# Optimization experiments

Hardware: AMD Instinct MI355X
Metric: run time of the kernel (lower is better)

Reference implementation:

```python
import jax, jax.numpy as jnp
import numpy as np

EXPERT_CAPACITY = 1024  # per-batch per-expert capacity (token_priority <= capacity)


def setup_inputs() -> dict:
    key = jax.random.key(0)
    ks = jax.random.split(key, 5)
    B, S, D, FF, E = 2, 4096, 1024, 4096, 8
    return {
        "hidden_states": jax.random.normal(ks[0], (B, S, D), dtype=jnp.float32),
        "gate_w": jax.random.normal(ks[1], (D, E), dtype=jnp.float32) * (1.0 / np.sqrt(D)),
        "w1": jax.random.normal(ks[2], (E, D, FF), dtype=jnp.float32) * (1.0 / np.sqrt(D)),
        "w2": jax.random.normal(ks[3], (E, FF, D), dtype=jnp.float32) * (1.0 / np.sqrt(FF)),
        "w3": jax.random.normal(ks[4], (E, D, FF), dtype=jnp.float32) * (1.0 / np.sqrt(D)),
    }


def reference(hidden_states, gate_w, w1, w2, w3):
    B, S, D = hidden_states.shape
    E = gate_w.shape[1]
    C = EXPERT_CAPACITY

    # ---- route (jitter_noise = 0) ----
    router_logits = jnp.einsum("bsd,de->bse", hidden_states, gate_w)  # [B,S,E]
    router_probs = jax.nn.softmax(router_logits, axis=-1)
    sel = jnp.argmax(router_probs, axis=-1)  # [B,S] top-1 expert
    onehot = jax.nn.one_hot(sel, E, dtype=jnp.int32)  # [B,S,E]
    priority = jnp.cumsum(onehot, axis=1)  # cumsum over sequence (dim=-2)
    # position of token in its chosen expert's buffer (0-based)
    pos = jnp.take_along_axis(priority, sel[..., None], axis=-1)[..., 0] - 1  # [B,S]
    keep = pos < C  # token_priority <= expert_capacity
    max_prob = jnp.max(router_probs, axis=-1, keepdims=True)  # [B,S,1]

    # ---- dispatch: scatter kept tokens into [B,E,C,D]; dropped tokens have pos>=C -> mode='drop'
    b_idx = jnp.broadcast_to(jnp.arange(B)[:, None], (B, S))
    buf = jnp.zeros((B, E, C, D), dtype=hidden_states.dtype)
    buf = buf.at[b_idx, sel, pos].set(hidden_states, mode="drop")

    # ---- per-expert gated MLP (grouped GEMM): act(x@w1) * (x@w3) @ w2 ----
    g = jax.nn.silu(jnp.einsum("becd,edf->becf", buf, w1))
    u = jnp.einsum("becd,edf->becf", buf, w3)
    expert_out = jnp.einsum("becf,efd->becd", g * u, w2)  # [B,E,C,D]

    # ---- combine: kept tokens get expert output, dropped tokens keep hidden_states ----
    pos_g = jnp.minimum(pos, C - 1)  # safe gather index for dropped tokens
    gathered = expert_out[b_idx, sel, pos_g]  # [B,S,D]
    next_states = jnp.where(keep[..., None], gathered, hidden_states)
    out = max_prob * next_states  # dropout is identity (p=0)
    return out, router_logits
```

## Files before the change

kernel.cpp:

```cpp
#include <hip/hip_runtime.h>
#include <hip/hip_bf16.h>
#include <stdint.h>

#define B_  2
#define S_  4096
#define D_  1024
#define FF_ 4096
#define E_  8
#define C_  1024

typedef unsigned short u16;
typedef unsigned int   u32;
typedef float f32x4  __attribute__((ext_vector_type(4)));
typedef short bf16x8 __attribute__((ext_vector_type(8)));
typedef u16   u16x8  __attribute__((ext_vector_type(8)));

static __device__ __forceinline__ u16 f2bf(float f) {
    union { float f; u32 u; } v; v.f = f;
    u32 u = v.u;
    u32 r = (u + 0x7FFFu + ((u >> 16) & 1u)) >> 16;
    return (u16)r;
}

static __device__ __forceinline__ void gload_lds16(const u16* g, u16* l) {
    __builtin_amdgcn_global_load_lds(
        (const __attribute__((address_space(1))) u32*)g,
        (__attribute__((address_space(3))) u32*)l, 16, 0, 0);
}

__global__ __launch_bounds__(256) void cvt_hidden(const float* __restrict__ src,
                                                  u16* __restrict__ dst, int n8) {
    int i = blockIdx.x * 256 + threadIdx.x;
    if (i >= n8) return;
    const float4* s = (const float4*)src + (size_t)i * 2;
    float4 a = s[0], b = s[1];
    u16x8 o;
    o[0] = f2bf(a.x); o[1] = f2bf(a.y); o[2] = f2bf(a.z); o[3] = f2bf(a.w);
    o[4] = f2bf(b.x); o[5] = f2bf(b.y); o[6] = f2bf(b.z); o[7] = f2bf(b.w);
    *((u16x8*)dst + i) = o;
}

__global__ __launch_bounds__(256) void transpose_cvt(const float* __restrict__ src,
                                                     u16* __restrict__ dst, int K, int N) {
    __shared__ float tile[32][33];
    size_t mat = (size_t)blockIdx.z * K * N;
    int n0 = blockIdx.x * 32, k0 = blockIdx.y * 32;
    int tx = threadIdx.x & 31, ty = threadIdx.x >> 5;
#pragma unroll
    for (int i = 0; i < 32; i += 8)
        tile[ty + i][tx] = src[mat + (size_t)(k0 + ty + i) * N + n0 + tx];
    __syncthreads();
#pragma unroll
    for (int i = 0; i < 32; i += 8)
        dst[mat + (size_t)(n0 + ty + i) * K + k0 + tx] = f2bf(tile[tx][ty + i]);
}

__global__ __launch_bounds__(256) void router_kernel(const float* __restrict__ hidden,
                                                     const float* __restrict__ gate_w,
                                                     float* __restrict__ logits_out,
                                                     int* __restrict__ sel,
                                                     float* __restrict__ maxp) {
    __shared__ float gw[D_ * E_];
    for (int i = threadIdx.x; i < D_ * E_ / 4; i += 256)
        ((float4*)gw)[i] = ((const float4*)gate_w)[i];
    __syncthreads();

    int wave = threadIdx.x >> 6, lane = threadIdx.x & 63;
    int tok = blockIdx.x * 4 + wave;
    const float* hrow = hidden + (size_t)tok * D_;

    double acc[8] = {0, 0, 0, 0, 0, 0, 0, 0};
#pragma unroll 4
    for (int i = 0; i < D_ / 64; i++) {
        int d = i * 64 + lane;
        float h = hrow[d];
        const float4* g4 = (const float4*)(gw + d * 8);
        float4 g0 = g4[0], g1 = g4[1];
        acc[0] += (double)h * g0.x; acc[1] += (double)h * g0.y;
        acc[2] += (double)h * g0.z; acc[3] += (double)h * g0.w;
        acc[4] += (double)h * g1.x; acc[5] += (double)h * g1.y;
        acc[6] += (double)h * g1.z; acc[7] += (double)h * g1.w;
    }
#pragma unroll
    for (int off = 32; off > 0; off >>= 1)
#pragma unroll
        for (int e = 0; e < 8; e++)
            acc[e] += __shfl_xor(acc[e], off);

    float l[8];
#pragma unroll
    for (int e = 0; e < 8; e++) l[e] = (float)acc[e];
    if (lane < 8) logits_out[(size_t)tok * 8 + lane] = l[lane];

    int am = 0; float mx = l[0];
#pragma unroll
    for (int e = 1; e < 8; e++) if (l[e] > mx) { mx = l[e]; am = e; }
    float sum = 0.f;
#pragma unroll
    for (int e = 0; e < 8; e++) sum += expf(l[e] - mx);
    if (lane == 0) { sel[tok] = am; maxp[tok] = 1.0f / sum; }
}

__global__ void scan_kernel(const int* __restrict__ sel, int* __restrict__ pos,
                            int* __restrict__ slot_token, int* __restrict__ counts) {
    int wave = threadIdx.x >> 6, lane = threadIdx.x & 63;
    int b = wave;
    int carry[8] = {0, 0, 0, 0, 0, 0, 0, 0};
    unsigned long long below = (lane == 0) ? 0ull : ((~0ull) >> (64 - lane));
    for (int s0 = 0; s0 < S_; s0 += 64) {
        int s = s0 + lane;
        int e = sel[b * S_ + s];
        int p = 0;
#pragma unroll
        for (int ex = 0; ex < 8; ex++) {
            unsigned long long m = __ballot(e == ex);
            if (e == ex) p = carry[ex] + (int)__popcll(m & below);
            carry[ex] += (int)__popcll(m);
        }
        pos[b * S_ + s] = p;
        if (p < C_) slot_token[(b * E_ + e) * C_ + p] = s;
    }
    if (lane < 8) {
        int c = carry[lane];
        counts[b * E_ + lane] = c < C_ ? c : C_;
    }
}

__global__ __launch_bounds__(256) void gemm1_kernel(const u16* __restrict__ x,
                                                    const u16* __restrict__ w1t,
                                                    const u16* __restrict__ w3t,
                                                    const int* __restrict__ slot_token,
                                                    const int* __restrict__ counts,
                                                    u16* __restrict__ hbuf) {
    int z = blockIdx.z;
    int cnt = counts[z];
    int c0 = blockIdx.y * 128;
    if (c0 >= cnt) return;
    int n0 = blockIdx.x * 64;
    int b = z >> 3, e = z & 7;

    __shared__ u16 As[128 * 64];
    __shared__ u16 B1s[64 * 64];
    __shared__ u16 B3s[64 * 64];

    int tid = threadIdx.x, wave = tid >> 6, lane = tid & 63;
    int wr = wave >> 1, wc = wave & 1;

    const u16* a_src[4];
#pragma unroll
    for (int i = 0; i < 4; i++) {
        int chunk = wave * 4 + i;
        int row = chunk * 8 + (lane >> 3);
        int slot = c0 + row;
        int s = (slot < cnt) ? slot_token[z * C_ + slot] : 0;
        int srcslot = (lane & 7) ^ (row & 7);
        a_src[i] = x + ((size_t)(b * S_ + s)) * D_ + srcslot * 8;
    }
    const u16 *b1_src[2], *b3_src[2];
#pragma unroll
    for (int i = 0; i < 2; i++) {
        int chunk = wave * 2 + i;
        int row = chunk * 8 + (lane >> 3);
        int srcslot = (lane & 7) ^ (row & 7);
        size_t off = ((size_t)e * FF_ + n0 + row) * D_ + srcslot * 8;
        b1_src[i] = w1t + off;
        b3_src[i] = w3t + off;
    }

    f32x4 acc1[4][2] = {};
    f32x4 acc3[4][2] = {};

    for (int k0 = 0; k0 < D_; k0 += 64) {
#pragma unroll
        for (int i = 0; i < 4; i++)
            gload_lds16(a_src[i] + k0, As + (wave * 4 + i) * 512);
#pragma unroll
        for (int i = 0; i < 2; i++) {
            gload_lds16(b1_src[i] + k0, B1s + (wave * 2 + i) * 512);
            gload_lds16(b3_src[i] + k0, B3s + (wave * 2 + i) * 512);
        }
        __syncthreads();
#pragma unroll
        for (int kk = 0; kk < 2; kk++) {
            bf16x8 af[4];
#pragma unroll
            for (int fm = 0; fm < 4; fm++) {
                int row = wr * 64 + fm * 16 + (lane & 15);
                int sl = (kk * 4 + (lane >> 4)) ^ (row & 7);
                af[fm] = *(const bf16x8*)(As + row * 64 + sl * 8);
            }
            bf16x8 b1f[2], b3f[2];
#pragma unroll
            for (int fn = 0; fn < 2; fn++) {
                int nl = wc * 32 + fn * 16 + (lane & 15);
                int sl = (kk * 4 + (lane >> 4)) ^ (nl & 7);
                b1f[fn] = *(const bf16x8*)(B1s + nl * 64 + sl * 8);
                b3f[fn] = *(const bf16x8*)(B3s + nl * 64 + sl * 8);
            }
#pragma unroll
            for (int fm = 0; fm < 4; fm++)
#pragma unroll
                for (int fn = 0; fn < 2; fn++) {
                    acc1[fm][fn] = __builtin_amdgcn_mfma_f32_16x16x32_bf16(af[fm], b1f[fn], acc1[fm][fn], 0, 0, 0);
                    acc3[fm][fn] = __builtin_amdgcn_mfma_f32_16x16x32_bf16(af[fm], b3f[fn], acc3[fm][fn], 0, 0, 0);
                }
        }
        __syncthreads();
    }

#pragma unroll
    for (int fm = 0; fm < 4; fm++) {
        int rbase = c0 + wr * 64 + fm * 16 + ((lane >> 4) << 2);
#pragma unroll
        for (int fn = 0; fn < 2; fn++) {
            int col = n0 + wc * 32 + fn * 16 + (lane & 15);
#pragma unroll
            for (int r = 0; r < 4; r++) {
                int slot = rbase + r;
                if (slot < cnt) {
                    float g = acc1[fm][fn][r];
                    float u = acc3[fm][fn][r];
                    float h = (g / (1.f + __expf(-g))) * u;
                    hbuf[((size_t)z * C_ + slot) * FF_ + col] = f2bf(h);
                }
            }
        }
    }
}

__global__ __launch_bounds__(256) void gemm2_kernel(const u16* __restrict__ hbuf,
                                                    const u16* __restrict__ w2t,
                                                    const int* __restrict__ slot_token,
                                                    const int* __restrict__ counts,
                                                    const float* __restrict__ maxp,
                                                    float* __restrict__ out) {
    int z = blockIdx.z;
    int cnt = counts[z];
    int c0 = blockIdx.y * 128;
    if (c0 >= cnt) return;
    int n0 = blockIdx.x * 128;
    int b = z >> 3, e = z & 7;

    __shared__ u16 As[128 * 64];
    __shared__ u16 Bs[128 * 64];

    int tid = threadIdx.x, wave = tid >> 6, lane = tid & 63;
    int wr = wave >> 1, wc = wave & 1;

    const u16 *a_src[4], *b_src[4];
#pragma unroll
    for (int i = 0; i < 4; i++) {
        int chunk = wave * 4 + i;
        int row = chunk * 8 + (lane >> 3);
        int srcslot = (lane & 7) ^ (row & 7);
        a_src[i] = hbuf + ((size_t)z * C_ + c0 + row) * FF_ + srcslot * 8;
        b_src[i] = w2t + ((size_t)e * D_ + n0 + row) * FF_ + srcslot * 8;
    }

    f32x4 acc[4][4] = {};

    for (int k0 = 0; k0 < FF_; k0 += 64) {
#pragma unroll
        for (int i = 0; i < 4; i++) {
            gload_lds16(a_src[i] + k0, As + (wave * 4 + i) * 512);
            gload_lds16(b_src[i] + k0, Bs + (wave * 4 + i) * 512);
        }
        __syncthreads();
#pragma unroll
        for (int kk = 0; kk < 2; kk++) {
            bf16x8 af[4], bfv[4];
#pragma unroll
            for (int fm = 0; fm < 4; fm++) {
                int row = wr * 64 + fm * 16 + (lane & 15);
                int sl = (kk * 4 + (lane >> 4)) ^ (row & 7);
                af[fm] = *(const bf16x8*)(As + row * 64 + sl * 8);
            }
#pragma unroll
            for (int fn = 0; fn < 4; fn++) {
                int nl = wc * 64 + fn * 16 + (lane & 15);
                int sl = (kk * 4 + (lane >> 4)) ^ (nl & 7);
                bfv[fn] = *(const bf16x8*)(Bs + nl * 64 + sl * 8);
            }
#pragma unroll
            for (int fm = 0; fm < 4; fm++)
#pragma unroll
                for (int fn = 0; fn < 4; fn++)
                    acc[fm][fn] = __builtin_amdgcn_mfma_f32_16x16x32_bf16(af[fm], bfv[fn], acc[fm][fn], 0, 0, 0);
        }
        __syncthreads();
    }

#pragma unroll
    for (int fm = 0; fm < 4; fm++) {
        int rbase = c0 + wr * 64 + fm * 16 + ((lane >> 4) << 2);
#pragma unroll
        for (int r = 0; r < 4; r++) {
            int slot = rbase + r;
            if (slot < cnt) {
                int s = slot_token[z * C_ + slot];
                float sc = maxp[b * S_ + s];
                float* orow = out + ((size_t)b * S_ + s) * D_;
#pragma unroll
                for (int fn = 0; fn < 4; fn++) {
                    int col = n0 + wc * 64 + fn * 16 + (lane & 15);
                    orow[col] = sc * acc[fm][fn][r];
                }
            }
        }
    }
}

__global__ __launch_bounds__(256) void combine_dropped(const float* __restrict__ hidden,
                                                       const int* __restrict__ pos,
                                                       const float* __restrict__ maxp,
                                                       float* __restrict__ out) {
    int t = blockIdx.x;
    if (pos[t] < C_) return;
    float sc = maxp[t];
    const float* src = hidden + (size_t)t * D_;
    float* dst = out + (size_t)t * D_;
    for (int d = threadIdx.x; d < D_; d += 256) dst[d] = sc * src[d];
}

extern "C" void kernel_launch(void* const* d_in, const int* in_sizes, int n_in,
                              void* d_out, int out_size, void* d_ws, size_t ws_size,
                              hipStream_t stream) {
    const float* hidden = (const float*)d_in[0];
    const float* gate_w = (const float*)d_in[1];
    const float* w1     = (const float*)d_in[2];
    const float* w2     = (const float*)d_in[3];
    const float* w3     = (const float*)d_in[4];

    float* out        = (float*)d_out;
    float* logits_out = out + (size_t)B_ * S_ * D_;

    char* ws = (char*)d_ws;
    u16* hidden_bf = (u16*)ws;            ws += (size_t)B_ * S_ * D_ * 2;
    u16* w1t       = (u16*)ws;            ws += (size_t)E_ * D_ * FF_ * 2;
    u16* w3t       = (u16*)ws;            ws += (size_t)E_ * D_ * FF_ * 2;
    u16* w2t       = (u16*)ws;            ws += (size_t)E_ * D_ * FF_ * 2;
    u16* hbuf      = (u16*)ws;            ws += (size_t)B_ * E_ * C_ * FF_ * 2;
    int*   sel        = (int*)ws;         ws += (size_t)B_ * S_ * 4;
    int*   pos        = (int*)ws;         ws += (size_t)B_ * S_ * 4;
    float* maxp       = (float*)ws;       ws += (size_t)B_ * S_ * 4;
    int*   slot_token = (int*)ws;         ws += (size_t)B_ * E_ * C_ * 4;
    int*   counts     = (int*)ws;         ws += (size_t)B_ * E_ * 4;

    cvt_hidden<<<(B_ * S_ * D_ / 8 + 255) / 256, 256, 0, stream>>>(hidden, hidden_bf, B_ * S_ * D_ / 8);
    transpose_cvt<<<dim3(FF_ / 32, D_ / 32, E_), 256, 0, stream>>>(w1, w1t, D_, FF_);
    transpose_cvt<<<dim3(FF_ / 32, D_ / 32, E_), 256, 0, stream>>>(w3, w3t, D_, FF_);
    transpose_cvt<<<dim3(D_ / 32, FF_ / 32, E_), 256, 0, stream>>>(w2, w2t, FF_, D_);

    router_kernel<<<B_ * S_ / 4, 256, 0, stream>>>(hidden, gate_w, logits_out, sel, maxp);
    scan_kernel<<<1, 128, 0, stream>>>(sel, pos, slot_token, counts);

    gemm1_kernel<<<dim3(FF_ / 64, C_ / 128, B_ * E_), 256, 0, stream>>>(hidden_bf, w1t, w3t, slot_token, counts, hbuf);
    gemm2_kernel<<<dim3(D_ / 128, C_ / 128, B_ * E_), 256, 0, stream>>>(hbuf, w2t, slot_token, counts, maxp, out);
    combine_dropped<<<B_ * S_, 256, 0, stream>>>(hidden, pos, maxp, out);
}
```

Before: 574.8 us.

## Double-buffer grouped GEMMs, widen gemm1 tile, fuse bf16 cast into router

Both expert GEMMs now use double-buffered LDS with a K-step of 32, prefetching the next stage before computing the current one. They sync with raw s_waitcnt and s_barrier and raise wave priority around the MFMA block. gemm1 widens its N tile from 64 to 128 to reuse each A tile more. The hidden-state bf16 conversion is folded into the router kernel, and the weight transpose uses 64x64 tiles with vectorized loads and stores and an XOR-swizzled LDS layout. The aim is to hide global-load latency, cut launches and improve transpose bandwidth, at the cost of more registers and LDS, which may reduce occupancy.

Result: slower. 609.5 us (+6.0%).

```diff
diff --git a/kernel.cpp b/kernel.cpp
--- a/kernel.cpp
+++ b/kernel.cpp
@@ -28,38 +28,48 @@
         (__attribute__((address_space(3))) u32*)l, 16, 0, 0);
 }
 
-__global__ __launch_bounds__(256) void cvt_hidden(const float* __restrict__ src,
-                                                  u16* __restrict__ dst, int n8) {
-    int i = blockIdx.x * 256 + threadIdx.x;
-    if (i >= n8) return;
-    const float4* s = (const float4*)src + (size_t)i * 2;
-    float4 a = s[0], b = s[1];
-    u16x8 o;
-    o[0] = f2bf(a.x); o[1] = f2bf(a.y); o[2] = f2bf(a.z); o[3] = f2bf(a.w);
-    o[4] = f2bf(b.x); o[5] = f2bf(b.y); o[6] = f2bf(b.z); o[7] = f2bf(b.w);
-    *((u16x8*)dst + i) = o;
-}
+#define BAR()    asm volatile("s_barrier" ::: "memory")
+#define WAITV(n) asm volatile("s_waitcnt vmcnt(" #n ")" ::: "memory")
 
 __global__ __launch_bounds__(256) void transpose_cvt(const float* __restrict__ src,
                                                      u16* __restrict__ dst, int K, int N) {
-    __shared__ float tile[32][33];
+    __shared__ u16 t[64 * 64];
     size_t mat = (size_t)blockIdx.z * K * N;
-    int n0 = blockIdx.x * 32, k0 = blockIdx.y * 32;
-    int tx = threadIdx.x & 31, ty = threadIdx.x >> 5;
-#pragma unroll
-    for (int i = 0; i < 32; i += 8)
-        tile[ty + i][tx] = src[mat + (size_t)(k0 + ty + i) * N + n0 + tx];
+    int n0 = blockIdx.x * 64, k0 = blockIdx.y * 64;
+    int l = threadIdx.x & 63, w = threadIdx.x >> 6;
+#pragma unroll
+    for (int p = 0; p < 2; ++p) {
+        int k = p * 32 + w * 8 + ((l >> 4) << 1);
+        int n = (l & 15) * 4;
+        float4 v0 = *(const float4*)&src[mat + (size_t)(k0 + k) * N + n0 + n];
+        float4 v1 = *(const float4*)&src[mat + (size_t)(k0 + k + 1) * N + n0 + n];
+        float a0[4] = {v0.x, v0.y, v0.z, v0.w};
+        float a1[4] = {v1.x, v1.y, v1.z, v1.w};
+#pragma unroll
+        for (int j = 0; j < 4; ++j) {
+            int nn = n + j;
+            u32 pk = (u32)f2bf(a0[j]) | ((u32)f2bf(a1[j]) << 16);
+            int slot = (k >> 3) ^ ((nn & 7) ^ ((nn >> 3) & 7));
+            *(u32*)((char*)t + nn * 128 + slot * 16 + (k & 7) * 2) = pk;
+        }
+    }
     __syncthreads();
 #pragma unroll
-    for (int i = 0; i < 32; i += 8)
-        dst[mat + (size_t)(n0 + ty + i) * K + k0 + tx] = f2bf(tile[tx][ty + i]);
+    for (int p = 0; p < 2; ++p) {
+        int n = p * 32 + (threadIdx.x >> 3);
+        int k8 = threadIdx.x & 7;
+        int slot = k8 ^ ((n & 7) ^ ((n >> 3) & 7));
+        u16x8 v = *(u16x8*)((char*)t + n * 128 + slot * 16);
+        *(u16x8*)&dst[mat + (size_t)(n0 + n) * K + k0 + k8 * 8] = v;
+    }
 }
 
 __global__ __launch_bounds__(256) void router_kernel(const float* __restrict__ hidden,
                                                      const float* __restrict__ gate_w,
                                                      float* __restrict__ logits_out,
                                                      int* __restrict__ sel,
-                                                     float* __restrict__ maxp) {
+                                                     float* __restrict__ maxp,
+                                                     u16* __restrict__ xbf) {
     __shared__ float gw[D_ * E_];
     for (int i = threadIdx.x; i < D_ * E_ / 4; i += 256)
         ((float4*)gw)[i] = ((const float4*)gate_w)[i];
@@ -68,12 +78,14 @@
     int wave = threadIdx.x >> 6, lane = threadIdx.x & 63;
     int tok = blockIdx.x * 4 + wave;
     const float* hrow = hidden + (size_t)tok * D_;
+    u16* xrow = xbf + (size_t)tok * D_;
 
     double acc[8] = {0, 0, 0, 0, 0, 0, 0, 0};
 #pragma unroll 4
     for (int i = 0; i < D_ / 64; i++) {
         int d = i * 64 + lane;
         float h = hrow[d];
+        xrow[d] = f2bf(h);
         const float4* g4 = (const float4*)(gw + d * 8);
         float4 g0 = g4[0], g1 = g4[1];
         acc[0] += (double)h * g0.x; acc[1] += (double)h * g0.y;
@@ -136,90 +148,99 @@
     int cnt = counts[z];
     int c0 = blockIdx.y * 128;
     if (c0 >= cnt) return;
-    int n0 = blockIdx.x * 64;
+    int n0 = blockIdx.x * 128;
     int b = z >> 3, e = z & 7;
 
-    __shared__ u16 As[128 * 64];
-    __shared__ u16 B1s[64 * 64];
-    __shared__ u16 B3s[64 * 64];
-
-    int tid = threadIdx.x, wave = tid >> 6, lane = tid & 63;
-    int wr = wave >> 1, wc = wave & 1;
-
-    const u16* a_src[4];
-#pragma unroll
-    for (int i = 0; i < 4; i++) {
-        int chunk = wave * 4 + i;
-        int row = chunk * 8 + (lane >> 3);
-        int slot = c0 + row;
-        int s = (slot < cnt) ? slot_token[z * C_ + slot] : 0;
-        int srcslot = (lane & 7) ^ (row & 7);
-        a_src[i] = x + ((size_t)(b * S_ + s)) * D_ + srcslot * 8;
-    }
-    const u16 *b1_src[2], *b3_src[2];
+    __shared__ u16 lds[2 * 12288];
+
+    int tid = threadIdx.x, w = tid >> 6, l = tid & 63;
+    int wr = w >> 1, wc = w & 1;
+
+    const u16 *aptr[2], *b1ptr[2], *b3ptr[2];
+    int sbase[2];
 #pragma unroll
     for (int i = 0; i < 2; i++) {
-        int chunk = wave * 2 + i;
-        int row = chunk * 8 + (lane >> 3);
-        int srcslot = (lane & 7) ^ (row & 7);
-        size_t off = ((size_t)e * FF_ + n0 + row) * D_ + srcslot * 8;
-        b1_src[i] = w1t + off;
-        b3_src[i] = w3t + off;
-    }
-
-    f32x4 acc1[4][2] = {};
-    f32x4 acc3[4][2] = {};
-
-    for (int k0 = 0; k0 < D_; k0 += 64) {
-#pragma unroll
-        for (int i = 0; i < 4; i++)
-            gload_lds16(a_src[i] + k0, As + (wave * 4 + i) * 512);
+        int rp = w * 16 + i * 8 + (l >> 3);
+        int ss = (l & 7) ^ (rp & 7);
+        int r  = 2 * rp + (ss >> 2);
+        int ko = (ss & 3) * 8;
+        int slot = c0 + r;
+        int tok = (slot < cnt) ? slot_token[z * C_ + slot] : 0;
+        aptr[i]  = x   + (size_t)(b * S_ + tok) * D_ + ko;
+        b1ptr[i] = w1t + ((size_t)e * FF_ + n0 + r) * D_ + ko;
+        b3ptr[i] = w3t + ((size_t)e * FF_ + n0 + r) * D_ + ko;
+        sbase[i] = (w * 16 + i * 8) * 64;
+    }
+
+    int afo[4], bfo[4];
+#pragma unroll
+    for (int f = 0; f < 4; f++) {
+        int rA = wr * 64 + f * 16 + (l & 15);
+        int rp = rA >> 1;
+        int ss = (rA & 1) * 4 + (l >> 4);
+        afo[f] = rp * 64 + (ss ^ (rp & 7)) * 8;
+        int nl = wc * 64 + f * 16 + (l & 15);
+        int rpb = nl >> 1;
+        int ssb = (nl & 1) * 4 + (l >> 4);
+        bfo[f] = rpb * 64 + (ssb ^ (rpb & 7)) * 8;
+    }
+
+    f32x4 acc1[4][4] = {};
+    f32x4 acc3[4][4] = {};
+
+    auto STAGE = [&](int buf, int t) {
+        u16* Ld = lds + buf * 12288;
+        int k0 = t * 32;
 #pragma unroll
         for (int i = 0; i < 2; i++) {
-            gload_lds16(b1_src[i] + k0, B1s + (wave * 2 + i) * 512);
-            gload_lds16(b3_src[i] + k0, B3s + (wave * 2 + i) * 512);
-        }
-        __syncthreads();
-#pragma unroll
-        for (int kk = 0; kk < 2; kk++) {
-            bf16x8 af[4];
-#pragma unroll
-            for (int fm = 0; fm < 4; fm++) {
-                int row = wr * 64 + fm * 16 + (lane & 15);
-                int sl = (kk * 4 + (lane >> 4)) ^ (row & 7);
-                af[fm] = *(const bf16x8*)(As + row * 64 + sl * 8);
+            gload_lds16(aptr[i]  + k0, Ld + sbase[i]);
+            gload_lds16(b1ptr[i] + k0, Ld + 4096 + sbase[i]);
+            gload_lds16(b3ptr[i] + k0, Ld + 8192 + sbase[i]);
+        }
+    };
+
+    constexpr int NT = D_ / 32;
+    STAGE(0, 0);
+    for (int t = 0; t < NT; ++t) {
+        int cur = t & 1;
+        if (t + 1 < NT) {
+            STAGE(cur ^ 1, t + 1);
+            WAITV(6);
+        } else {
+            WAITV(0);
+        }
+        BAR();
+        const u16* Lc = lds + cur * 12288;
+        bf16x8 af[4], b1f[4], b3f[4];
+#pragma unroll
+        for (int f = 0; f < 4; f++) af[f]  = *(const bf16x8*)(Lc + afo[f]);
+#pragma unroll
+        for (int f = 0; f < 4; f++) b1f[f] = *(const bf16x8*)(Lc + 4096 + bfo[f]);
+#pragma unroll
+        for (int f = 0; f < 4; f++) b3f[f] = *(const bf16x8*)(Lc + 8192 + bfo[f]);
+        __builtin_amdgcn_s_setprio(1);
+#pragma unroll
+        for (int fm = 0; fm < 4; fm++)
+#pragma unroll
+            for (int fn = 0; fn < 4; fn++) {
+                acc1[fm][fn] = __builtin_amdgcn_mfma_f32_16x16x32_bf16(af[fm], b1f[fn], acc1[fm][fn], 0, 0, 0);
+                acc3[fm][fn] = __builtin_amdgcn_mfma_f32_16x16x32_bf16(af[fm], b3f[fn], acc3[fm][fn], 0, 0, 0);
             }
-            bf16x8 b1f[2], b3f[2];
-#pragma unroll
-            for (int fn = 0; fn < 2; fn++) {
-                int nl = wc * 32 + fn * 16 + (lane & 15);
-                int sl = (kk * 4 + (lane >> 4)) ^ (nl & 7);
-                b1f[fn] = *(const bf16x8*)(B1s + nl * 64 + sl * 8);
-                b3f[fn] = *(const bf16x8*)(B3s + nl * 64 + sl * 8);
-            }
-#pragma unroll
-            for (int fm = 0; fm < 4; fm++)
-#pragma unroll
-                for (int fn = 0; fn < 2; fn++) {
-                    acc1[fm][fn] = __builtin_amdgcn_mfma_f32_16x16x32_bf16(af[fm], b1f[fn], acc1[fm][fn], 0, 0, 0);
-                    acc3[fm][fn] = __builtin_amdgcn_mfma_f32_16x16x32_bf16(af[fm], b3f[fn], acc3[fm][fn], 0, 0, 0);
-                }
-        }
-        __syncthreads();
+        __builtin_amdgcn_s_setprio(0);
+        BAR();
     }
 
 #pragma unroll
     for (int fm = 0; fm < 4; fm++) {
-        int rbase = c0 + wr * 64 + fm * 16 + ((lane >> 4) << 2);
-#pragma unroll
-        for (int fn = 0; fn < 2; fn++) {
-            int col = n0 + wc * 32 + fn * 16 + (lane & 15);
+        int rb = c0 + wr * 64 + fm * 16 + ((l >> 4) << 2);
+#pragma unroll
+        for (int fn = 0; fn < 4; fn++) {
+            int col = n0 + wc * 64 + fn * 16 + (l & 15);
 #pragma unroll
             for (int r = 0; r < 4; r++) {
-                int slot = rbase + r;
+                int slot = rb + r;
                 if (slot < cnt) {
-                    float g = acc1[fm][fn][r];
-                    float u = acc3[fm][fn][r];
+                    float g = acc1[fm][fn][r], u = acc3[fm][fn][r];
                     float h = (g / (1.f + __expf(-g))) * u;
                     hbuf[((size_t)z * C_ + slot) * FF_ + col] = f2bf(h);
                 }
@@ -241,68 +262,89 @@
     int n0 = blockIdx.x * 128;
     int b = z >> 3, e = z & 7;
 
-    __shared__ u16 As[128 * 64];
-    __shared__ u16 Bs[128 * 64];
-
-    int tid = threadIdx.x, wave = tid >> 6, lane = tid & 63;
-    int wr = wave >> 1, wc = wave & 1;
-
-    const u16 *a_src[4], *b_src[4];
-#pragma unroll
-    for (int i = 0; i < 4; i++) {
-        int chunk = wave * 4 + i;
-        int row = chunk * 8 + (lane >> 3);
-        int srcslot = (lane & 7) ^ (row & 7);
-        a_src[i] = hbuf + ((size_t)z * C_ + c0 + row) * FF_ + srcslot * 8;
-        b_src[i] = w2t + ((size_t)e * D_ + n0 + row) * FF_ + srcslot * 8;
+    __shared__ u16 lds[2 * 8192];
+
+    int tid = threadIdx.x, w = tid >> 6, l = tid & 63;
+    int wr = w >> 1, wc = w & 1;
+
+    const u16 *aptr[2], *bptr[2];
+    int sbase[2];
+#pragma unroll
+    for (int i = 0; i < 2; i++) {
+        int rp = w * 16 + i * 8 + (l >> 3);
+        int ss = (l & 7) ^ (rp & 7);
+        int r  = 2 * rp + (ss >> 2);
+        int ko = (ss & 3) * 8;
+        aptr[i] = hbuf + ((size_t)z * C_ + c0 + r) * FF_ + ko;
+        bptr[i] = w2t + ((size_t)e * D_ + n0 + r) * FF_ + ko;
+        sbase[i] = (w * 16 + i * 8) * 64;
+    }
+
+    int afo[4], bfo[4];
+#pragma unroll
+    for (int f = 0; f < 4; f++) {
+        int rA = wr * 64 + f * 16 + (l & 15);
+        int rp = rA >> 1;
+        int ss = (rA & 1) * 4 + (l >> 4);
+        afo[f] = rp * 64 + (ss ^ (rp & 7)) * 8;
+        int nl = wc * 64 + f * 16 + (l & 15);
+        int rpb = nl >> 1;
+        int ssb = (nl & 1) * 4 + (l >> 4);
+        bfo[f] = rpb * 64 + (ssb ^ (rpb & 7)) * 8;
     }
 
     f32x4 acc[4][4] = {};
 
-    for (int k0 = 0; k0 < FF_; k0 += 64) {
-#pragma unroll
-        for (int i = 0; i < 4; i++) {
-            gload_lds16(a_src[i] + k0, As + (wave * 4 + i) * 512);
-            gload_lds16(b_src[i] + k0, Bs + (wave * 4 + i) * 512);
-        }
-        __syncthreads();
-#pragma unroll
-        for (int kk = 0; kk < 2; kk++) {
-            bf16x8 af[4], bfv[4];
-#pragma unroll
-            for (int fm = 0; fm < 4; fm++) {
-                int row = wr * 64 + fm * 16 + (lane & 15);
-                int sl = (kk * 4 + (lane >> 4)) ^ (row & 7);
-                af[fm] = *(const bf16x8*)(As + row * 64 + sl * 8);
-            }
-#pragma unroll
-            for (int fn = 0; fn < 4; fn++) {
-                int nl = wc * 64 + fn * 16 + (lane & 15);
-                int sl = (kk * 4 + (lane >> 4)) ^ (nl & 7);
-                bfv[fn] = *(const bf16x8*)(Bs + nl * 64 + sl * 8);
-            }
-#pragma unroll
-            for (int fm = 0; fm < 4; fm++)
-#pragma unroll
-                for (int fn = 0; fn < 4; fn++)
-                    acc[fm][fn] = __builtin_amdgcn_mfma_f32_16x16x32_bf16(af[fm], bfv[fn], acc[fm][fn], 0, 0, 0);
-        }
-        __syncthreads();
+    auto STAGE = [&](int buf, int t) {
+        u16* Ld = lds + buf * 8192;
+        int k0 = t * 32;
+#pragma unroll
+        for (int i = 0; i < 2; i++) {
+            gload_lds16(aptr[i] + k0, Ld + sbase[i]);
+            gload_lds16(bptr[i] + k0, Ld + 4096 + sbase[i]);
+        }
+    };
+
+    constexpr int NT = FF_ / 32;
+    STAGE(0, 0);
+    for (int t = 0; t < NT; ++t) {
+        int cur = t & 1;
+        if (t + 1 < NT) {
+            STAGE(cur ^ 1, t + 1);
+            WAITV(4);
+        } else {
+            WAITV(0);
+        }
+        BAR();
+        const u16* Lc = lds + cur * 8192;
+        bf16x8 af[4], bfv[4];
+#pragma unroll
+        for (int f = 0; f < 4; f++) af[f]  = *(const bf16x8*)(Lc + afo[f]);
+#pragma unroll
+        for (int f = 0; f < 4; f++) bfv[f] = *(const bf16x8*)(Lc + 4096 + bfo[f]);
+        __builtin_amdgcn_s_setprio(1);
+#pragma unroll
+        for (int fm = 0; fm < 4; fm++)
+#pragma unroll
+            for (int fn = 0; fn < 4; fn++)
+                acc[fm][fn] = __builtin_amdgcn_mfma_f32_16x16x32_bf16(af[fm], bfv[fn], acc[fm][fn], 0, 0, 0);
+        __builtin_amdgcn_s_setprio(0);
+        BAR();
     }
 
 #pragma unroll
     for (int fm = 0; fm < 4; fm++) {
-        int rbase = c0 + wr * 64 + fm * 16 + ((lane >> 4) << 2);
+        int rb = c0 + wr * 64 + fm * 16 + ((l >> 4) << 2);
 #pragma unroll
         for (int r = 0; r < 4; r++) {
-            int slot = rbase + r;
+            int slot = rb + r;
             if (slot < cnt) {
                 int s = slot_token[z * C_ + slot];
                 float sc = maxp[b * S_ + s];
                 float* orow = out + ((size_t)b * S_ + s) * D_;
 #pragma unroll
                 for (int fn = 0; fn < 4; fn++) {
-                    int col = n0 + wc * 64 + fn * 16 + (lane & 15);
+                    int col = n0 + wc * 64 + fn * 16 + (l & 15);
                     orow[col] = sc * acc[fm][fn][r];
                 }
             }
@@ -346,15 +388,14 @@
     int*   slot_token = (int*)ws;         ws += (size_t)B_ * E_ * C_ * 4;
     int*   counts     = (int*)ws;         ws += (size_t)B_ * E_ * 4;
 
-    cvt_hidden<<<(B_ * S_ * D_ / 8 + 255) / 256, 256, 0, stream>>>(hidden, hidden_bf, B_ * S_ * D_ / 8);
-    transpose_cvt<<<dim3(FF_ / 32, D_ / 32, E_), 256, 0, stream>>>(w1, w1t, D_, FF_);
-    transpose_cvt<<<dim3(FF_ / 32, D_ / 32, E_), 256, 0, stream>>>(w3, w3t, D_, FF_);
-    transpose_cvt<<<dim3(D_ / 32, FF_ / 32, E_), 256, 0, stream>>>(w2, w2t, FF_, D_);
-
-    router_kernel<<<B_ * S_ / 4, 256, 0, stream>>>(hidden, gate_w, logits_out, sel, maxp);
+    router_kernel<<<B_ * S_ / 4, 256, 0, stream>>>(hidden, gate_w, logits_out, sel, maxp, hidden_bf);
     scan_kernel<<<1, 128, 0, stream>>>(sel, pos, slot_token, counts);
 
-    gemm1_kernel<<<dim3(FF_ / 64, C_ / 128, B_ * E_), 256, 0, stream>>>(hidden_bf, w1t, w3t, slot_token, counts, hbuf);
+    transpose_cvt<<<dim3(FF_ / 64, D_ / 64, E_), 256, 0, stream>>>(w1, w1t, D_, FF_);
+    transpose_cvt<<<dim3(FF_ / 64, D_ / 64, E_), 256, 0, stream>>>(w3, w3t, D_, FF_);
+    transpose_cvt<<<dim3(D_ / 64, FF_ / 64, E_), 256, 0, stream>>>(w2, w2t, FF_, D_);
+
+    gemm1_kernel<<<dim3(FF_ / 128, C_ / 128, B_ * E_), 256, 0, stream>>>(hidden_bf, w1t, w3t, slot_token, counts, hbuf);
     gemm2_kernel<<<dim3(D_ / 128, C_ / 128, B_ * E_), 256, 0, stream>>>(hbuf, w2t, slot_token, counts, maxp, out);
     combine_dropped<<<B_ * S_, 256, 0, stream>>>(hidden, pos, maxp, out);
 }
```
